# Kernel optimization log

Hardware: AMD Instinct MI355X
Metric: run time of the kernel (lower is better)

## Reference

```python
import jax, jax.numpy as jnp
import numpy as np
from jax import lax

INF = 1e6  # stand-in for infinity; INF**2 = 1e12 fits comfortably in fp32


def _boundary_3x3(targets):
    """morphological_gradient(size=(3,3)) > 0 on int label maps [B,H,W].
    scipy default mode='reflect' with pad width 1 == edge padding."""
    B, H, W = targets.shape
    p = jnp.pad(targets, ((0, 0), (1, 1), (1, 1)), mode='edge')
    patches = jnp.stack([p[:, i:i + H, j:j + W]
                         for i in range(3) for j in range(3)], axis=0)
    return (patches.max(0) - patches.min(0)) > 0  # [B,H,W] bool


def _row_dist(boundary):
    """Per-row 1D distance (in column index) to nearest boundary pixel. [B,H,W] float."""
    B, H, W = boundary.shape
    bT = jnp.moveaxis(boundary, 2, 0)  # [W,B,H]

    def step(c, b):
        c = jnp.where(b, 0.0, jnp.minimum(c + 1.0, INF))
        return c, c

    init = jnp.full((B, H), INF, dtype=jnp.float32)
    _, fwd = lax.scan(step, init, bT)
    _, bwd = lax.scan(step, init, bT[::-1])
    g = jnp.minimum(fwd, bwd[::-1])  # [W,B,H]
    return jnp.moveaxis(g, 0, 2)  # [B,H,W]


def _edt(boundary):
    """Exact 2D Euclidean distance transform to the boundary set (separable form):
    d(i,j)^2 = min_k ( (i-k)^2 + g(k,j)^2 )."""
    B, H, W = boundary.shape
    g2 = _row_dist(boundary) ** 2  # [B,H,W]
    ii = jnp.arange(H, dtype=jnp.float32)
    dk2 = (ii[:, None] - ii[None, :]) ** 2  # [H_i, H_k]
    # [B, H_i, H_k, W] -> min over k
    d2 = jnp.min(dk2[None, :, :, None] + g2[:, None, :, :], axis=2)
    return jnp.sqrt(d2)


def boundary_weight(targets, sigma):
    boundary = _boundary_3x3(targets)
    dist = _edt(boundary)
    w = jnp.exp(-dist / sigma)
    has_b = boundary.any(axis=(1, 2))[:, None, None]
    return jnp.where(has_b, w, 1.0)  # all-ones map if no boundary


def setup_inputs() -> dict:
    key = jax.random.key(0)
    k1, k2 = jax.random.split(key)
    B, C, H, W = 8, 19, 256, 256
    inputs = jax.random.normal(k1, (B, C, H, W), dtype=jnp.float32)
    targets = jax.random.randint(k2, (B, H, W), 0, C, dtype=jnp.int32)
    return {"inputs": inputs, "targets": targets}


def reference(inputs, targets):
    sigma = 5.0
    logp = jax.nn.log_softmax(inputs, axis=1)  # [B,C,H,W]
    ce = -jnp.take_along_axis(logp, targets[:, None, :, :], axis=1)[:, 0]  # [B,H,W]
    w = boundary_weight(targets, sigma)
    return (ce * w).mean()
```

## Files before the change

### kernel.cpp

```cpp
#include <hip/hip_runtime.h>

#define BB 8
#define CC 19
#define HH 256
#define WW 256
#define HWW 65536
#define IT 8
#define BIGF 3.0e12f


__global__ __launch_bounds__(256) void k_bnd_ce(
    const float* __restrict__ x, const int* __restrict__ tgt,
    float* __restrict__ g2, float* __restrict__ ce,
    int* __restrict__ rowany, float* __restrict__ out)
{
    const int blk = blockIdx.x;
    const int b   = blk >> 6;
    const int i0  = (blk & 63) << 2;
    const int j   = threadIdx.x;

    __shared__ int trow[6][WW];
    __shared__ int bflag[4][WW];
    __shared__ int s_any;

    if (blk == 0 && j == 0) out[0] = 0.0f;
    if (j == 0) s_any = 0;

    const int r  = j >> 6;
    const int c0 = (j & 63) << 2;
    const int h  = i0 + r;

    const float* px = x + ((size_t)(b * CC) * HH + h) * WW + c0;
    float4 v[CC];
#pragma unroll
    for (int c = 0; c < CC; ++c)
        v[c] = *(const float4*)(px + (size_t)c * HWW);

    const int* tbase = tgt + b * HWW;
#pragma unroll
    for (int rr = 0; rr < 6; ++rr) {
        int hh = min(max(i0 - 1 + rr, 0), HH - 1);
        trow[rr][j] = tbase[hh * WW + j];
    }
    __syncthreads();

    int anyb = 0;
#pragma unroll
    for (int t = 0; t < 4; ++t) {
        int c = c0 + t;
        int cm = max(c - 1, 0), cp = min(c + 1, WW - 1);
        int mx = trow[r][cm], mn = mx;
#pragma unroll
        for (int rr = 0; rr < 3; ++rr) {
            int a0 = trow[r + rr][cm], a1 = trow[r + rr][c], a2 = trow[r + rr][cp];
            mx = max(mx, max(a0, max(a1, a2)));
            mn = min(mn, min(a0, min(a1, a2)));
        }
        int bnd = (mx != mn) ? 1 : 0;
        bflag[r][c] = bnd;
        anyb |= bnd;
    }
    unsigned long long msk = __ballot(anyb);
    if ((j & 63) == 0 && msk) s_any = 1;
    __syncthreads();
    if (j == 0) rowany[blk] = s_any;

    float4 g4;
    float* gp = (float*)&g4;
#pragma unroll
    for (int t = 0; t < 4; ++t) {
        int c = c0 + t;
        float mind = 1e6f;
        for (int d = 0; d < WW; ++d) {
            int lo = c - d, hi = c + d;
            if ((lo >= 0 && bflag[r][lo]) || (hi < WW && bflag[r][hi])) {
                mind = (float)d; break;
            }
        }
        gp[t] = mind * mind;
    }
    *(float4*)(g2 + (size_t)(b * HH + h) * WW + c0) = g4;

    float4 s4 = make_float4(0.f, 0.f, 0.f, 0.f);
#pragma unroll
    for (int c = 0; c < CC; ++c) {
        s4.x += expf(v[c].x); s4.y += expf(v[c].y);
        s4.z += expf(v[c].z); s4.w += expf(v[c].w);
    }
    const int t0 = trow[r + 1][c0],     t1 = trow[r + 1][c0 + 1],
              t2 = trow[r + 1][c0 + 2], t3 = trow[r + 1][c0 + 3];
    float4 c4;
    c4.x = logf(s4.x) - px[(size_t)t0 * HWW + 0];
    c4.y = logf(s4.y) - px[(size_t)t1 * HWW + 1];
    c4.z = logf(s4.z) - px[(size_t)t2 * HWW + 2];
    c4.w = logf(s4.w) - px[(size_t)t3 * HWW + 3];
    *(float4*)(ce + (size_t)(b * HH + h) * WW + c0) = c4;
}

__global__ __launch_bounds__(256) void k_edt_red(
    const float* __restrict__ g2, const float* __restrict__ ce,
    const int* __restrict__ rowany, float* __restrict__ out)
{
    const int b  = blockIdx.x >> 5;
    const int i0 = (blockIdx.x & 31) * IT;
    const int j  = threadIdx.x;

    __shared__ int s_has;
    __shared__ float wsum[4];
    if (j == 0) s_has = 0;
    int ra = (j < 64) ? rowany[b * 64 + j] : 0;
    unsigned long long mk = __ballot(ra != 0);
    __syncthreads();
    if ((j & 63) == 0 && mk) s_has = 1;
    __syncthreads();
    const int has = s_has;

    float md[IT];
#pragma unroll
    for (int r = 0; r < IT; ++r) md[r] = BIGF;
    const float* gcol = g2 + (size_t)b * HWW + j;
    const int c0 = i0 + 4;
    for (int d0 = 0; d0 < HH; d0 += 4) {
        float gl[4], gr[4];
        int   kl[4], kr[4];
#pragma unroll
        for (int t = 0; t < 4; ++t) {
            int d = d0 + t;
            kl[t] = c0 - d; kr[t] = c0 + d;
            gl[t] = (kl[t] >= 0 && kl[t] < HH) ? gcol[(size_t)kl[t] * WW] : BIGF;
            gr[t] = (kr[t] >= 0 && kr[t] < HH) ? gcol[(size_t)kr[t] * WW] : BIGF;
        }
#pragma unroll
        for (int t = 0; t < 4; ++t) {
#pragma unroll
            for (int r = 0; r < IT; ++r) {
                float dl = (float)(i0 + r - kl[t]);
                float dr = (float)(i0 + r - kr[t]);
                md[r] = fminf(md[r], fmaf(dl, dl, gl[t]));
                md[r] = fminf(md[r], fmaf(dr, dr, gr[t]));
            }
        }
        float bm = md[0];
#pragma unroll
        for (int r = 1; r < IT; ++r) bm = fmaxf(bm, md[r]);
        float fut = (float)(d0 * d0);
        if (fut > bm) break;
    }

    float acc = 0.0f;
#pragma unroll
    for (int r = 0; r < IT; ++r) {
        float dist = sqrtf(md[r]);
        float w = has ? expf(-dist / 5.0f) : 1.0f;
        acc += ce[((size_t)b * HH + i0 + r) * WW + j] * w;
    }

    for (int off = 32; off > 0; off >>= 1)
        acc += __shfl_down(acc, off, 64);
    const int lane = j & 63, wid = j >> 6;
    if (lane == 0) wsum[wid] = acc;
    __syncthreads();
    if (j == 0) {
        float tot = wsum[0] + wsum[1] + wsum[2] + wsum[3];
        atomicAdd(out, tot * (1.0f / (float)(BB * HWW)));
    }
}

extern "C" void kernel_launch(void* const* d_in, const int* in_sizes, int n_in,
                              void* d_out, int out_size, void* d_ws, size_t ws_size,
                              hipStream_t stream) {
    const float* x   = (const float*)d_in[0];
    const int*   tgt = (const int*)d_in[1];
    float*       out = (float*)d_out;

    char* ws = (char*)d_ws;
    float* g2     = (float*)ws;
    float* ce     = (float*)(ws + (size_t)BB * HWW * sizeof(float));
    int*   rowany = (int*)  (ws + (size_t)2 * BB * HWW * sizeof(float));

    k_bnd_ce <<<BB * (HH / 4), 256, 0, stream>>>(x, tgt, g2, ce, rowany, out);
    k_edt_red<<<BB * (HH / IT), 256, 0, stream>>>(g2, ce, rowany, out);
}
```

Before: 89.04 us.

## Fuse boundary/CE and EDT kernels into one cooperative kernel with grid sync

```diff
diff --git a/kernel.cpp b/kernel.cpp
--- a/kernel.cpp
+++ b/kernel.cpp
@@ -1,40 +1,39 @@
 #include <hip/hip_runtime.h>
+#include <hip/hip_cooperative_groups.h>
+
+namespace cg = cooperative_groups;
 
 #define BB 8
 #define CC 19
 #define HH 256
 #define WW 256
 #define HWW 65536
-#define IT 8
+#define NBLK 512
+#define POISON 0xAAAAAAAAu
 #define BIGF 3.0e12f
 
 
-__global__ __launch_bounds__(256) void k_bnd_ce(
+__global__ __launch_bounds__(256, 2) void k_all(
     const float* __restrict__ x, const int* __restrict__ tgt,
-    float* __restrict__ g2, float* __restrict__ ce,
-    int* __restrict__ rowany, float* __restrict__ out)
+    float* __restrict__ g2, int* __restrict__ rowany,
+    unsigned* __restrict__ gbar, float* __restrict__ partials,
+    float* __restrict__ out)
 {
     const int blk = blockIdx.x;
     const int b   = blk >> 6;
     const int i0  = (blk & 63) << 2;
     const int j   = threadIdx.x;
+    const int r   = j >> 6;
+    const int c0  = (j & 63) << 2;
+    const int h   = i0 + r;
 
-    __shared__ int trow[6][WW];
-    __shared__ int bflag[4][WW];
-    __shared__ int s_any;
+    __shared__ int   trow[6][WW];
+    __shared__ int   bflag[4][WW];
+    __shared__ float s_w[4][WW];
+    __shared__ int   s_any, s_has, s_last;
+    __shared__ float wsum[4];
 
-    if (blk == 0 && j == 0) out[0] = 0.0f;
-    if (j == 0) s_any = 0;
-
-    const int r  = j >> 6;
-    const int c0 = (j & 63) << 2;
-    const int h  = i0 + r;
-
-    const float* px = x + ((size_t)(b * CC) * HH + h) * WW + c0;
-    float4 v[CC];
-#pragma unroll
-    for (int c = 0; c < CC; ++c)
-        v[c] = *(const float4*)(px + (size_t)c * HWW);
+    if (j == 0) { s_any = 0; s_last = 0; atomicCAS(gbar, POISON, 0u); }
 
     const int* tbase = tgt + b * HWW;
 #pragma unroll
@@ -47,7 +46,7 @@
     int anyb = 0;
 #pragma unroll
     for (int t = 0; t < 4; ++t) {
-        int c = c0 + t;
+        int c  = c0 + t;
         int cm = max(c - 1, 0), cp = min(c + 1, WW - 1);
         int mx = trow[r][cm], mn = mx;
 #pragma unroll
@@ -65,8 +64,7 @@
     __syncthreads();
     if (j == 0) rowany[blk] = s_any;
 
-    float4 g4;
-    float* gp = (float*)&g4;
+    float4 g4; float* gp = (float*)&g4;
 #pragma unroll
     for (int t = 0; t < 4; ++t) {
         int c = c0 + t;
@@ -81,6 +79,53 @@
     }
     *(float4*)(g2 + (size_t)(b * HH + h) * WW + c0) = g4;
 
+    __threadfence();
+    cg::this_grid().sync();
+
+    int ra = (j < 64) ? rowany[b * 64 + j] : 0;
+    unsigned long long mk = __ballot(ra != 0);
+    if (j == 0) s_has = 0;
+    __syncthreads();
+    if ((j & 63) == 0 && mk) s_has = 1;
+    __syncthreads();
+    const int has = s_has;
+
+    float md[4] = {BIGF, BIGF, BIGF, BIGF};
+    const float* gcol = g2 + (size_t)b * HWW + j;
+    const int ctr = i0 + 2;
+    for (int d0 = 0; d0 < HH; d0 += 4) {
+        float gl[4], gr[4]; int kl[4], kr[4];
+#pragma unroll
+        for (int t = 0; t < 4; ++t) {
+            int d = d0 + t;
+            kl[t] = ctr - d; kr[t] = ctr + d;
+            gl[t] = (kl[t] >= 0 && kl[t] < HH) ? gcol[(size_t)kl[t] * WW] : BIGF;
+            gr[t] = (kr[t] >= 0 && kr[t] < HH) ? gcol[(size_t)kr[t] * WW] : BIGF;
+        }
+#pragma unroll
+        for (int t = 0; t < 4; ++t) {
+#pragma unroll
+            for (int rr = 0; rr < 4; ++rr) {
+                float dl = (float)(i0 + rr - kl[t]);
+                float dr = (float)(i0 + rr - kr[t]);
+                md[rr] = fminf(md[rr], fmaf(dl, dl, gl[t]));
+                md[rr] = fminf(md[rr], fmaf(dr, dr, gr[t]));
+            }
+        }
+        float bm = fmaxf(fmaxf(md[0], md[1]), fmaxf(md[2], md[3]));
+        float fut = (float)((d0 + 2) * (d0 + 2));
+        if (fut > bm) break;
+    }
+#pragma unroll
+    for (int rr = 0; rr < 4; ++rr)
+        s_w[rr][j] = has ? expf(-sqrtf(md[rr]) / 5.0f) : 1.0f;
+    __syncthreads();
+
+    const float* px = x + ((size_t)(b * CC) * HH + h) * WW + c0;
+    float4 v[CC];
+#pragma unroll
+    for (int c = 0; c < CC; ++c)
+        v[c] = *(const float4*)(px + (size_t)c * HWW);
     float4 s4 = make_float4(0.f, 0.f, 0.f, 0.f);
 #pragma unroll
     for (int c = 0; c < CC; ++c) {
@@ -89,71 +134,11 @@
     }
     const int t0 = trow[r + 1][c0],     t1 = trow[r + 1][c0 + 1],
               t2 = trow[r + 1][c0 + 2], t3 = trow[r + 1][c0 + 3];
-    float4 c4;
-    c4.x = logf(s4.x) - px[(size_t)t0 * HWW + 0];
-    c4.y = logf(s4.y) - px[(size_t)t1 * HWW + 1];
-    c4.z = logf(s4.z) - px[(size_t)t2 * HWW + 2];
-    c4.w = logf(s4.w) - px[(size_t)t3 * HWW + 3];
-    *(float4*)(ce + (size_t)(b * HH + h) * WW + c0) = c4;
-}
-
-__global__ __launch_bounds__(256) void k_edt_red(
-    const float* __restrict__ g2, const float* __restrict__ ce,
-    const int* __restrict__ rowany, float* __restrict__ out)
-{
-    const int b  = blockIdx.x >> 5;
-    const int i0 = (blockIdx.x & 31) * IT;
-    const int j  = threadIdx.x;
-
-    __shared__ int s_has;
-    __shared__ float wsum[4];
-    if (j == 0) s_has = 0;
-    int ra = (j < 64) ? rowany[b * 64 + j] : 0;
-    unsigned long long mk = __ballot(ra != 0);
-    __syncthreads();
-    if ((j & 63) == 0 && mk) s_has = 1;
-    __syncthreads();
-    const int has = s_has;
-
-    float md[IT];
-#pragma unroll
-    for (int r = 0; r < IT; ++r) md[r] = BIGF;
-    const float* gcol = g2 + (size_t)b * HWW + j;
-    const int c0 = i0 + 4;
-    for (int d0 = 0; d0 < HH; d0 += 4) {
-        float gl[4], gr[4];
-        int   kl[4], kr[4];
-#pragma unroll
-        for (int t = 0; t < 4; ++t) {
-            int d = d0 + t;
-            kl[t] = c0 - d; kr[t] = c0 + d;
-            gl[t] = (kl[t] >= 0 && kl[t] < HH) ? gcol[(size_t)kl[t] * WW] : BIGF;
-            gr[t] = (kr[t] >= 0 && kr[t] < HH) ? gcol[(size_t)kr[t] * WW] : BIGF;
-        }
-#pragma unroll
-        for (int t = 0; t < 4; ++t) {
-#pragma unroll
-            for (int r = 0; r < IT; ++r) {
-                float dl = (float)(i0 + r - kl[t]);
-                float dr = (float)(i0 + r - kr[t]);
-                md[r] = fminf(md[r], fmaf(dl, dl, gl[t]));
-                md[r] = fminf(md[r], fmaf(dr, dr, gr[t]));
-            }
-        }
-        float bm = md[0];
-#pragma unroll
-        for (int r = 1; r < IT; ++r) bm = fmaxf(bm, md[r]);
-        float fut = (float)(d0 * d0);
-        if (fut > bm) break;
-    }
-
-    float acc = 0.0f;
-#pragma unroll
-    for (int r = 0; r < IT; ++r) {
-        float dist = sqrtf(md[r]);
-        float w = has ? expf(-dist / 5.0f) : 1.0f;
-        acc += ce[((size_t)b * HH + i0 + r) * WW + j] * w;
-    }
+    float4 ww = *(const float4*)&s_w[r][c0];
+    float acc = (logf(s4.x) - px[(size_t)t0 * HWW + 0]) * ww.x
+              + (logf(s4.y) - px[(size_t)t1 * HWW + 1]) * ww.y
+              + (logf(s4.z) - px[(size_t)t2 * HWW + 2]) * ww.z
+              + (logf(s4.w) - px[(size_t)t3 * HWW + 3]) * ww.w;
 
     for (int off = 32; off > 0; off >>= 1)
         acc += __shfl_down(acc, off, 64);
@@ -161,8 +146,21 @@
     if (lane == 0) wsum[wid] = acc;
     __syncthreads();
     if (j == 0) {
-        float tot = wsum[0] + wsum[1] + wsum[2] + wsum[3];
-        atomicAdd(out, tot * (1.0f / (float)(BB * HWW)));
+        partials[blk] = wsum[0] + wsum[1] + wsum[2] + wsum[3];
+        __threadfence();
+        unsigned old = atomicAdd(gbar, 1u);
+        if (old == NBLK - 1) { __threadfence(); s_last = 1; }
+    }
+    __syncthreads();
+    if (s_last) {
+        float p = partials[j] + partials[j + 256];
+        for (int off = 32; off > 0; off >>= 1)
+            p += __shfl_down(p, off, 64);
+        if (lane == 0) wsum[wid] = p;
+        __syncthreads();
+        if (j == 0)
+            out[0] = (wsum[0] + wsum[1] + wsum[2] + wsum[3])
+                   * (1.0f / (float)(BB * HWW));
     }
 }
 
@@ -174,10 +172,12 @@
     float*       out = (float*)d_out;
 
     char* ws = (char*)d_ws;
-    float* g2     = (float*)ws;
-    float* ce     = (float*)(ws + (size_t)BB * HWW * sizeof(float));
-    int*   rowany = (int*)  (ws + (size_t)2 * BB * HWW * sizeof(float));
+    unsigned* gbar     = (unsigned*)ws;
+    float*    partials = (float*)(ws + 64);
+    int*      rowany   = (int*)(ws + 4096);
+    float*    g2       = (float*)(ws + 8192);
 
-    k_bnd_ce <<<BB * (HH / 4), 256, 0, stream>>>(x, tgt, g2, ce, rowany, out);
-    k_edt_red<<<BB * (HH / IT), 256, 0, stream>>>(g2, ce, rowany, out);
+    void* args[] = { (void*)&x, (void*)&tgt, (void*)&g2, (void*)&rowany,
+                     (void*)&gbar, (void*)&partials, (void*)&out };
+    hipLaunchCooperativeKernel((void*)k_all, dim3(NBLK), dim3(256), args, 0, stream);
 }
```

Measured after the change: 184.2 us. 107% more time.
